# Kernel tuning notes

Measured on AMD Instinct MI355X. Metric: run time of the kernel, lower is better.

## Reference

```python
import jax, jax.numpy as jnp
import numpy as np

N, E = 25000, 400000
IN, HID, OUT = 128, 256, 128
T = 4                      # towers
F1, F2 = HID // T, OUT // T  # per-tower out dims (divide_input=False)
A = 12                     # len(aggregators)=4 * len(scalers)=3
EPS_STD = 1e-5
EPS_BN = 1e-5


def _glorot(k, shape):
    fin, fout = shape[-2], shape[-1]
    lim = float(np.sqrt(6.0 / (fin + fout)))
    return jax.random.uniform(k, shape, jnp.float32, -lim, lim)


def setup_inputs():
    key = jax.random.key(0)
    ks = jax.random.split(key, 10)
    x = jax.random.normal(ks[0], (N, IN), jnp.float32)
    edge_index = jax.random.randint(ks[1], (2, E), 0, N, dtype=jnp.int32)
    # avg_deg['log'] buffer of PNAConv: mean over nodes of log(deg+1)
    deg = jax.ops.segment_sum(jnp.ones((E,), jnp.float32), edge_index[1], num_segments=N)
    avg_log = jnp.mean(jnp.log(deg + 1.0)).astype(jnp.float32)
    return dict(
        x=x, edge_index=edge_index, avg_log=avg_log,
        pre1_W=_glorot(ks[2], (T, 2 * IN, F1)), pre1_b=jnp.zeros((T, F1), jnp.float32),
        post1_W=_glorot(ks[3], (T, IN + A * F1, F1)), post1_b=jnp.zeros((T, F1), jnp.float32),
        lin1_W=_glorot(ks[4], (T * F1, HID)), lin1_b=jnp.zeros((HID,), jnp.float32),
        bn1_g=jnp.ones((HID,), jnp.float32), bn1_b=jnp.zeros((HID,), jnp.float32),
        pre2_W=_glorot(ks[5], (T, 2 * HID, F2)), pre2_b=jnp.zeros((T, F2), jnp.float32),
        post2_W=_glorot(ks[6], (T, HID + A * F2, F2)), post2_b=jnp.zeros((T, F2), jnp.float32),
        lin2_W=_glorot(ks[7], (T * F2, OUT)), lin2_b=jnp.zeros((OUT,), jnp.float32),
        bn2_g=jnp.ones((OUT,), jnp.float32), bn2_b=jnp.zeros((OUT,), jnp.float32),
    )


def _pna(x, src, tgt, preW, preB, postW, postB, linW, linB, avg_log):
    """PNAConv: towers=T, divide_input=False, pre_layers=post_layers=1,
    aggregators [mean,min,max,std], scalers [identity,amplification,attenuation]."""
    n = x.shape[0]
    # message: per tower Linear on concat([x_i, x_j]) where i=target, j=source
    h = jnp.concatenate([x[tgt], x[src]], axis=-1)            # [E, 2*F_in]
    msg = jnp.einsum('ec,tcf->etf', h, preW) + preB           # [E, T, F]
    ones = jnp.ones((msg.shape[0],), msg.dtype)
    deg = jax.ops.segment_sum(ones, tgt, num_segments=n)      # in-degree [n]
    degc = jnp.maximum(deg, 1.0)[:, None, None]
    s1 = jax.ops.segment_sum(msg, tgt, num_segments=n)
    mean = s1 / degc
    s2 = jax.ops.segment_sum(msg * msg, tgt, num_segments=n)
    var = jnp.maximum(s2 / degc - mean * mean, 0.0)
    std = jnp.sqrt(var + EPS_STD)
    has = (deg > 0.0)[:, None, None]
    mn = jnp.where(has, jax.ops.segment_min(msg, tgt, num_segments=n), 0.0)
    mx = jnp.where(has, jax.ops.segment_max(msg, tgt, num_segments=n), 0.0)
    agg = jnp.concatenate([mean, mn, mx, std], axis=-1)       # [n, T, 4F]
    dlog = jnp.log(jnp.maximum(deg, 1.0) + 1.0)[:, None, None]
    out = jnp.concatenate([agg, agg * (dlog / avg_log), agg * (avg_log / dlog)], axis=-1)  # [n, T, 12F]
    xt = jnp.broadcast_to(x[:, None, :], (n, T, x.shape[-1]))
    post_in = jnp.concatenate([xt, out], axis=-1)             # [n, T, F_in + 12F]
    post = jnp.einsum('ntc,tcf->ntf', post_in, postW) + postB # [n, T, F]
    return post.reshape(n, -1) @ linW + linB                  # [n, out]


def _bn(x, g, b):
    # BatchNorm1d training-mode math: biased batch variance
    m = jnp.mean(x, axis=0)
    v = jnp.mean((x - m) ** 2, axis=0)
    return g * (x - m) / jnp.sqrt(v + EPS_BN) + b


def reference(x, edge_index, avg_log, pre1_W, pre1_b, post1_W, post1_b, lin1_W, lin1_b,
              bn1_g, bn1_b, pre2_W, pre2_b, post2_W, post2_b, lin2_W, lin2_b, bn2_g, bn2_b):
    src, tgt = edge_index[0], edge_index[1]
    h = _pna(x, src, tgt, pre1_W, pre1_b, post1_W, post1_b, lin1_W, lin1_b, avg_log)
    h = jax.nn.relu(_bn(jnp.nan_to_num(h), bn1_g, bn1_b))
    h = _pna(h, src, tgt, pre2_W, pre2_b, post2_W, post2_b, lin2_W, lin2_b, avg_log)
    h = jax.nn.relu(_bn(jnp.nan_to_num(h), bn2_g, bn2_b))
    return h
```

## Files before the change

kernel.cpp:

```cpp
#include <hip/hip_runtime.h>
#include <hip/hip_bf16.h>
#include <float.h>
#include <math.h>

typedef __hip_bfloat16 bf16;
typedef __attribute__((ext_vector_type(8))) short short8;
typedef __attribute__((ext_vector_type(4))) float f32x4;

__device__ __forceinline__ float bf2f(bf16 v){ return __bfloat162float(v); }
__device__ __forceinline__ void stv(float* p, float v){ *p = v; }
__device__ __forceinline__ void stv(bf16* p, float v){ *p = __float2bfloat16(v); }
__device__ __forceinline__ float nanfix(float v){
  if (v != v) return 0.f;
  return fminf(fmaxf(v, -FLT_MAX), FLT_MAX);
}
__device__ __forceinline__ unsigned short f2bu(float f){
  unsigned u = __float_as_uint(f);
  unsigned r = u + 0x7FFFu + ((u>>16)&1u);
  return (unsigned short)(r>>16);
}
template<int VEC>
__device__ __forceinline__ void ldbf(const bf16* p, float (&o)[VEC]){
  if constexpr (VEC==4){
    ushort4 r = *(const ushort4*)p;
    o[0]=__uint_as_float((unsigned)r.x<<16); o[1]=__uint_as_float((unsigned)r.y<<16);
    o[2]=__uint_as_float((unsigned)r.z<<16); o[3]=__uint_as_float((unsigned)r.w<<16);
  } else {
    ushort2 r = *(const ushort2*)p;
    o[0]=__uint_as_float((unsigned)r.x<<16); o[1]=__uint_as_float((unsigned)r.y<<16);
  }
}

__global__ void k_scan1(const int* __restrict__ deg, int* __restrict__ bsum, int N){
  __shared__ int sm[256];
  int i = blockIdx.x*256 + threadIdx.x;
  sm[threadIdx.x] = (i < N) ? deg[i] : 0;
  __syncthreads();
  for (int off = 128; off > 0; off >>= 1){
    if (threadIdx.x < off) sm[threadIdx.x] += sm[threadIdx.x + off];
    __syncthreads();
  }
  if (threadIdx.x == 0) bsum[blockIdx.x] = sm[0];
}

__global__ void k_scan2(int* __restrict__ bsum, int NB){
  __shared__ int sm[1024];
  int tid = threadIdx.x;
  sm[tid] = (tid < NB) ? bsum[tid] : 0;
  __syncthreads();
  for (int off = 1; off < 1024; off <<= 1){
    int t = (tid >= off) ? sm[tid-off] : 0;
    __syncthreads();
    sm[tid] += t;
    __syncthreads();
  }
  if (tid < NB) bsum[tid] = (tid == 0) ? 0 : sm[tid-1];
}

__global__ void k_scan3(const int* __restrict__ deg, const int* __restrict__ bsum,
                        int* __restrict__ offs, int N){
  __shared__ int sm[256];
  int tid = threadIdx.x;
  int i = blockIdx.x*256 + tid;
  int v = (i < N) ? deg[i] : 0;
  sm[tid] = v; __syncthreads();
  for (int off = 1; off < 256; off <<= 1){
    int t = (tid >= off) ? sm[tid-off] : 0;
    __syncthreads();
    sm[tid] += t;
    __syncthreads();
  }
  if (i < N) offs[i+1] = bsum[blockIdx.x] + sm[tid];
  if (i == 0) offs[0] = 0;
}

__global__ void k_scatter(const int* __restrict__ src, const int* __restrict__ tgt,
                          const int* __restrict__ offs, int* __restrict__ cnt,
                          int* __restrict__ ssrc, int E){
  int e = blockIdx.x*blockDim.x + threadIdx.x;
  if (e < E){
    int t = tgt[e];
    int pos = offs[t] + atomicAdd(&cnt[t], 1);
    ssrc[pos] = src[e];
  }
}

__device__ __forceinline__ void rp_pqT(const float* preW, const float* preB,
                                       bf16* WpqT, float* bpq, int K, int F, int idx){
  int NC = 4*F;
  int total = 2*NC*K;
  if (idx < total){
    int j = idx/K, c = idx%K;
    int half = j/NC, jj = j%NC, t = jj/F, f = jj%F;
    WpqT[idx] = __float2bfloat16(preW[(t*2*K + half*K + c)*F + f]);
  }
  if (idx < 2*NC) bpq[idx] = (idx < NC) ? preB[idx] : 0.f;
}
__device__ __forceinline__ void rp_xT(const float* postW, const float* postB,
                                      bf16* WxT, float* bpost, int KX, int F, int idx){
  int NC = 4*F; int KP = KX + 12*F;
  if (idx < NC*KX){
    int j = idx/KX, c = idx%KX, t = j/F, f = j%F;
    WxT[idx] = __float2bfloat16(postW[(t*KP + c)*F + f]);
  }
  if (idx < NC) bpost[idx] = postB[idx];
}
__device__ __forceinline__ void rp_agg3(const float* postW, bf16* Wagg3,
                                        int KX, int F, int idx){
  int K4F = 4*F; int KP = KX + 12*F;
  int total = 4*3*F*K4F;
  if (idx < total){
    int k = idx % K4F; int r = idx / K4F;
    int zr = r % (3*F); int t = r / (3*F);
    int s = zr / F, f = zr % F;
    Wagg3[idx] = __float2bfloat16(postW[((size_t)(t*KP + KX + s*K4F + k))*F + f]);
  }
}
__device__ __forceinline__ void rp_linT(const float* linW, bf16* WlinT,
                                        int K, int NC, int idx){
  if (idx < NC*K){
    int j = idx/K, c = idx%K;
    WlinT[idx] = __float2bfloat16(linW[c*NC + j]);
  }
}

struct SetupArgs {
  const float *pre1W, *pre1b, *post1W, *post1b, *lin1W;
  const float *pre2W, *pre2b, *post2W, *post2b, *lin2W;
  const float *x;
  const int *tgt;
  bf16 *WpqT1, *WxT1, *Wagg31, *lin1WT;
  bf16 *WpqT2, *WxT2, *Wagg32, *lin2WT;
  bf16 *x_bf;
  int *deg;
  float *bpq1, *bpost1, *bpq2, *bpost2;
  int nx4;
  int E;
  int gstride;
};

__global__ void k_setup(SetupArgs a){
  int idx = blockIdx.x*256 + threadIdx.x;
  switch (blockIdx.y){
    case 0: rp_pqT (a.pre1W, a.pre1b, a.WpqT1, a.bpq1, 128, 64, idx); break;
    case 1: rp_xT  (a.post1W, a.post1b, a.WxT1, a.bpost1, 128, 64, idx); break;
    case 2: rp_agg3(a.post1W, a.Wagg31, 128, 64, idx); break;
    case 3: rp_linT(a.lin1W, a.lin1WT, 256, 256, idx); break;
    case 4: rp_pqT (a.pre2W, a.pre2b, a.WpqT2, a.bpq2, 256, 32, idx); break;
    case 5: rp_xT  (a.post2W, a.post2b, a.WxT2, a.bpost2, 256, 32, idx); break;
    case 6: rp_agg3(a.post2W, a.Wagg32, 256, 32, idx); break;
    case 7: rp_linT(a.lin2W, a.lin2WT, 128, 128, idx); break;
    case 8:
      for (int i = idx; i < a.nx4; i += a.gstride){
        float4 v = *(const float4*)(a.x + (size_t)i*4);
        ushort4 o = make_ushort4(f2bu(v.x), f2bu(v.y), f2bu(v.z), f2bu(v.w));
        *(ushort4*)(a.x_bf + (size_t)i*4) = o;
      }
      break;
    case 9:
      for (int e = idx; e < a.E; e += a.gstride)
        atomicAdd(&a.deg[a.tgt[e]], 1);
      break;
  }
}

template<typename TO, bool STATS>
__global__ __launch_bounds__(256) void k_mgemm(
    const bf16* __restrict__ A, int lda,
    const bf16* __restrict__ Bt,
    const float* __restrict__ bias,
    TO* __restrict__ Cout, int ldc,
    int N, int K, int NC, float* __restrict__ part)
{
  __shared__ __align__(16) bf16 As[64*40];
  __shared__ __align__(16) bf16 Bs[64*40];
  __shared__ float sstat[4][2][16][2];
  int n0 = blockIdx.y*64;
  int j0 = blockIdx.x*64;
  int tid = threadIdx.x;
  int srow = tid>>2, skoff = (tid&3)*8;
  int wave = tid>>6, lane = tid&63;
  int wy = (wave>>1)*32, wx = (wave&1)*32;
  int l15 = lane&15, q = lane>>4;
  f32x4 acc[2][2] = {};
  for (int k0 = 0; k0 < K; k0 += 32){
    uint4 av = {0,0,0,0};
    int ar = n0 + srow;
    if (ar < N) av = *(const uint4*)(A + (size_t)ar*lda + k0 + skoff);
    *(uint4*)&As[srow*40 + skoff] = av;
    uint4 bv = {0,0,0,0};
    int br = j0 + srow;
    if (br < NC) bv = *(const uint4*)(Bt + (size_t)br*K + k0 + skoff);
    *(uint4*)&Bs[srow*40 + skoff] = bv;
    __syncthreads();
    short8 af[2], bfr[2];
    #pragma unroll
    for (int i = 0; i < 2; i++){
      af[i]  = *(const short8*)&As[(wy + i*16 + l15)*40 + q*8];
      bfr[i] = *(const short8*)&Bs[(wx + i*16 + l15)*40 + q*8];
    }
    #pragma unroll
    for (int mi = 0; mi < 2; mi++)
      #pragma unroll
      for (int ni = 0; ni < 2; ni++)
        acc[mi][ni] = __builtin_amdgcn_mfma_f32_16x16x32_bf16(af[mi], bfr[ni], acc[mi][ni], 0, 0, 0);
    __syncthreads();
  }
  float cs[2] = {0.f, 0.f}, cq[2] = {0.f, 0.f};
  #pragma unroll
  for (int mi = 0; mi < 2; mi++){
    #pragma unroll
    for (int ni = 0; ni < 2; ni++){
      #pragma unroll
      for (int r = 0; r < 4; r++){
        int n  = n0 + wy + mi*16 + q*4 + r;
        int jj = j0 + wx + ni*16 + l15;
        if (n < N && jj < NC){
          float v = acc[mi][ni][r] + bias[jj];
          stv(&Cout[(size_t)n*ldc + jj], v);
          if constexpr (STATS){ cs[ni] += v; cq[ni] = fmaf(v, v, cq[ni]); }
        }
      }
    }
  }
  if constexpr (STATS){
    #pragma unroll
    for (int ni = 0; ni < 2; ni++){
      float s = cs[ni], qq = cq[ni];
      s  += __shfl_xor(s, 16);  s  += __shfl_xor(s, 32);
      qq += __shfl_xor(qq, 16); qq += __shfl_xor(qq, 32);
      if (q == 0){ sstat[wave][ni][l15][0] = s; sstat[wave][ni][l15][1] = qq; }
    }
    __syncthreads();
    if (tid < 64){
      int j = tid;
      int wa = (j < 32) ? 0 : 1, wb = wa + 2;
      int ni = (j & 31) >> 4, li = j & 15;
      float s  = sstat[wa][ni][li][0] + sstat[wb][ni][li][0];
      float qq = sstat[wa][ni][li][1] + sstat[wb][ni][li][1];
      part[(size_t)blockIdx.y*2*ldc + (j0 + j)]       = s;
      part[(size_t)blockIdx.y*2*ldc + ldc + (j0 + j)] = qq;
    }
  }
}

template<int COLS>
__global__ __launch_bounds__(256) void k_postagg(
    const bf16* __restrict__ agg,
    const bf16* __restrict__ Wagg3,
    const bf16* __restrict__ PQX, int ldq, int cinOff,
    const float* __restrict__ scal,
    bf16* __restrict__ Cout, int ldc, int N)
{
  constexpr int K4F = 4*COLS;
  constexpr int ROWS3 = 3*COLS;
  constexpr int NI = COLS/32;
  constexpr int LDA_AGG = 16*COLS;
  __shared__ __align__(16) bf16 As[64*40];
  __shared__ __align__(16) bf16 Bs[ROWS3*40];
  int z = blockIdx.z;
  int n0 = blockIdx.y*64;
  int tid = threadIdx.x;
  int srow = tid>>2, skoff = (tid&3)*8;
  int wave = tid>>6, lane = tid&63;
  int wy = (wave>>1)*32;
  int wx = (wave&1)*(COLS/2);
  int l15 = lane&15, q = lane>>4;
  f32x4 acc[2][NI][3] = {};
  const bf16* Az = agg + (size_t)z*K4F;
  const bf16* Bz = Wagg3 + (size_t)z*ROWS3*K4F;
  for (int k0 = 0; k0 < K4F; k0 += 32){
    uint4 av = {0,0,0,0};
    int ar = n0 + srow;
    if (ar < N) av = *(const uint4*)(Az + (size_t)ar*LDA_AGG + k0 + skoff);
    *(uint4*)&As[srow*40 + skoff] = av;
    for (int r = srow; r < ROWS3; r += 64){
      uint4 bv = *(const uint4*)(Bz + (size_t)r*K4F + k0 + skoff);
      *(uint4*)&Bs[r*40 + skoff] = bv;
    }
    __syncthreads();
    short8 af[2];
    #pragma unroll
    for (int i = 0; i < 2; i++)
      af[i] = *(const short8*)&As[(wy + i*16 + l15)*40 + q*8];
    #pragma unroll
    for (int s = 0; s < 3; s++){
      #pragma unroll
      for (int ni = 0; ni < NI; ni++){
        short8 bfr = *(const short8*)&Bs[(s*COLS + wx + ni*16 + l15)*40 + q*8];
        #pragma unroll
        for (int mi = 0; mi < 2; mi++)
          acc[mi][ni][s] = __builtin_amdgcn_mfma_f32_16x16x32_bf16(af[mi], bfr, acc[mi][ni][s], 0, 0, 0);
      }
    }
    __syncthreads();
  }
  #pragma unroll
  for (int mi = 0; mi < 2; mi++){
    #pragma unroll
    for (int ni = 0; ni < NI; ni++){
      int jj = wx + ni*16 + l15;
      int jg = z*COLS + jj;
      #pragma unroll
      for (int r = 0; r < 4; r++){
        int n = n0 + wy + mi*16 + q*4 + r;
        if (n < N){
          float s1 = scal[2*n], s2 = scal[2*n+1];
          float cin = bf2f(PQX[(size_t)n*ldq + cinOff + jg]);
          float v = cin + acc[mi][ni][0][r] + s1*acc[mi][ni][1][r] + s2*acc[mi][ni][2][r];
          Cout[(size_t)n*ldc + jg] = __float2bfloat16(v);
        }
      }
    }
  }
}

template<int NC, int F>
__global__ __launch_bounds__(256) void k_agg(const bf16* __restrict__ PQ, int lda,
    const int* __restrict__ ssrc, const int* __restrict__ offs,
    const float* __restrict__ avgp,
    bf16* __restrict__ agg, float* __restrict__ scal, int N){
  constexpr int VEC = NC/64;
  int wave = threadIdx.x>>6, lane = threadIdx.x&63;
  int n = blockIdx.x*4 + wave;
  if (n >= N) return;
  int c0 = lane*VEC;
  float p[VEC];
  ldbf<VEC>(PQ + (size_t)n*lda + c0, p);
  int s0 = offs[n], s1 = offs[n+1];
  float sum[VEC], sq[VEC], mn[VEC], mx[VEC];
  #pragma unroll
  for (int v=0;v<VEC;v++){ sum[v]=0.f; sq[v]=0.f; mn[v]=FLT_MAX; mx[v]=-FLT_MAX; }
  const bf16* Q = PQ + NC + c0;
  int i = s0;
  for (; i+7 < s1; i += 8){
    int se[8];
    #pragma unroll
    for (int u=0;u<8;u++) se[u] = ssrc[i+u];
    float qv[8][VEC];
    #pragma unroll
    for (int u=0;u<8;u++) ldbf<VEC>(Q + (size_t)se[u]*lda, qv[u]);
    #pragma unroll
    for (int u=0;u<8;u++){
      #pragma unroll
      for (int v=0;v<VEC;v++){
        float qq = qv[u][v];
        sum[v] += qq; sq[v] = fmaf(qq,qq,sq[v]);
        mn[v] = fminf(mn[v], qq); mx[v] = fmaxf(mx[v], qq);
      }
    }
  }
  for (; i+3 < s1; i += 4){
    int se[4];
    #pragma unroll
    for (int u=0;u<4;u++) se[u] = ssrc[i+u];
    float qv[4][VEC];
    #pragma unroll
    for (int u=0;u<4;u++) ldbf<VEC>(Q + (size_t)se[u]*lda, qv[u]);
    #pragma unroll
    for (int u=0;u<4;u++){
      #pragma unroll
      for (int v=0;v<VEC;v++){
        float qq = qv[u][v];
        sum[v] += qq; sq[v] = fmaf(qq,qq,sq[v]);
        mn[v] = fminf(mn[v], qq); mx[v] = fmaxf(mx[v], qq);
      }
    }
  }
  for (; i < s1; i++){
    int sa = ssrc[i];
    float qa[VEC];
    ldbf<VEC>(Q + (size_t)sa*lda, qa);
    #pragma unroll
    for (int v=0;v<VEC;v++){
      float qq = qa[v];
      sum[v]+=qq; sq[v]=fmaf(qq,qq,sq[v]); mn[v]=fminf(mn[v],qq); mx[v]=fmaxf(mx[v],qq);
    }
  }
  int deg = s1-s0;
  float degf = (float)deg;
  float degc = fmaxf(degf, 1.f);
  unsigned short um[VEC], un[VEC], ux[VEC], us[VEC];
  #pragma unroll
  for (int v=0;v<VEC;v++){
    float pv = p[v];
    float sum_m = fmaf(degf, pv, sum[v]);
    float sq_m  = sq[v] + 2.f*pv*sum[v] + degf*pv*pv;
    float mean = sum_m/degc;
    float var = fmaxf(sq_m/degc - mean*mean, 0.f);
    float sd = sqrtf(var + 1e-5f);
    float mnv = deg>0 ? pv + mn[v] : 0.f;
    float mxv = deg>0 ? pv + mx[v] : 0.f;
    um[v]=f2bu(mean); un[v]=f2bu(mnv); ux[v]=f2bu(mxv); us[v]=f2bu(sd);
  }
  int t = c0 / F, f0 = c0 % F;
  bf16* base = agg + (size_t)n*4*NC + (size_t)t*4*F + f0;
  if constexpr (VEC==4){
    *(ushort4*)(base)       = make_ushort4(um[0],um[1],um[2],um[3]);
    *(ushort4*)(base + F)   = make_ushort4(un[0],un[1],un[2],un[3]);
    *(ushort4*)(base + 2*F) = make_ushort4(ux[0],ux[1],ux[2],ux[3]);
    *(ushort4*)(base + 3*F) = make_ushort4(us[0],us[1],us[2],us[3]);
  } else {
    *(ushort2*)(base)       = make_ushort2(um[0],um[1]);
    *(ushort2*)(base + F)   = make_ushort2(un[0],un[1]);
    *(ushort2*)(base + 2*F) = make_ushort2(ux[0],ux[1]);
    *(ushort2*)(base + 3*F) = make_ushort2(us[0],us[1]);
  }
  if (lane==0){
    float dlog = logf(degc + 1.f);
    float avg = *avgp;
    scal[2*n]   = dlog/avg;
    scal[2*n+1] = avg/dlog;
  }
}

template<int C>
__global__ __launch_bounds__(256) void k_bn_final(const float* __restrict__ part, int PB,
                                                  float* __restrict__ stats){
  int c = blockIdx.x*256 + threadIdx.x;
  if (c >= 2*C) return;
  int CH = gridDim.y;
  int per = (PB + CH - 1)/CH;
  int p0 = blockIdx.y*per, p1 = min(p0 + per, PB);
  float acc = 0.f;
  int p = p0;
  for (; p+4 <= p1; p += 4){
    acc += part[(size_t)p*2*C + c] + part[(size_t)(p+1)*2*C + c]
         + part[(size_t)(p+2)*2*C + c] + part[(size_t)(p+3)*2*C + c];
  }
  for (; p < p1; p++) acc += part[(size_t)p*2*C + c];
  atomicAdd(&stats[c], acc);
}

template<typename TO, int C>
__global__ void k_bn_apply(const bf16* __restrict__ h, const float* __restrict__ stats,
     const float* __restrict__ g, const float* __restrict__ b,
     TO* __restrict__ out, int N){
  int idx = blockIdx.x*blockDim.x + threadIdx.x;
  if (idx >= N*(C/4)) return;
  int c = (idx % (C/4))*4;
  float fn = (float)N;
  float v[4];
  ldbf<4>(h + (size_t)idx*4, v);
  float r[4];
  #pragma unroll
  for (int k = 0; k < 4; k++){
    float m = stats[c+k]/fn;
    float var = fmaxf(stats[C+c+k]/fn - m*m, 0.f);
    float inv = rsqrtf(var + 1e-5f);
    float vv = nanfix(v[k]);
    r[k] = fmaxf(g[c+k]*(vv - m)*inv + b[c+k], 0.f);
  }
  if constexpr (sizeof(TO) == 4){
    float4 o = {r[0], r[1], r[2], r[3]};
    *(float4*)((float*)out + (size_t)idx*4) = o;
  } else {
    ushort4 o = make_ushort4(f2bu(r[0]), f2bu(r[1]), f2bu(r[2]), f2bu(r[3]));
    *(ushort4*)((bf16*)out + (size_t)idx*4) = o;
  }
}

static inline int cdiv(int a, int b){ return (a + b - 1)/b; }

extern "C" void kernel_launch(void* const* d_in, const int* in_sizes, int n_in,
                              void* d_out, int out_size, void* d_ws, size_t ws_size,
                              hipStream_t stream){
  const int IN = 128, HID = 256, T = 4, F1 = 64, F2 = 32;
  const int N = in_sizes[0]/IN;
  const int E = in_sizes[1]/2;
  const int NC1 = T*F1;
  const int NC2 = T*F2;
  const int LDQ1 = 2*NC1 + NC1;
  const int LDQ2 = 2*NC2 + NC2;

  const float* x      = (const float*)d_in[0];
  const int*   ei     = (const int*)  d_in[1];
  const int*   srcE   = ei;
  const int*   tgtE   = ei + E;
  const float* avgp   = (const float*)d_in[2];
  const float* pre1W  = (const float*)d_in[3];
  const float* pre1b  = (const float*)d_in[4];
  const float* post1W = (const float*)d_in[5];
  const float* post1b = (const float*)d_in[6];
  const float* lin1W  = (const float*)d_in[7];
  const float* lin1b  = (const float*)d_in[8];
  const float* bn1g   = (const float*)d_in[9];
  const float* bn1b   = (const float*)d_in[10];
  const float* pre2W  = (const float*)d_in[11];
  const float* pre2b  = (const float*)d_in[12];
  const float* post2W = (const float*)d_in[13];
  const float* post2b = (const float*)d_in[14];
  const float* lin2W  = (const float*)d_in[15];
  const float* lin2b  = (const float*)d_in[16];
  const float* bn2g   = (const float*)d_in[17];
  const float* bn2b   = (const float*)d_in[18];

  char* w = (char*)d_ws;
  auto alloc = [&](size_t bytes)->void*{
    void* p = (void*)w; w += (bytes + 255) & ~(size_t)255; return p;
  };
  bf16* BT1    = (bf16*)alloc((size_t)LDQ1*IN*2);
  bf16* WpqT1  = BT1;              bf16* WxT1 = BT1 + (size_t)2*NC1*IN;
  float* bias1 = (float*)alloc((size_t)LDQ1*4);
  float* bpq1  = bias1;            float* bpost1 = bias1 + 2*NC1;
  bf16* Wagg31 = (bf16*)alloc((size_t)T*3*F1*4*F1*2);
  bf16* lin1WT = (bf16*)alloc((size_t)HID*NC1*2);
  bf16* BT2    = (bf16*)alloc((size_t)LDQ2*HID*2);
  bf16* WpqT2  = BT2;              bf16* WxT2 = BT2 + (size_t)2*NC2*HID;
  float* bias2 = (float*)alloc((size_t)LDQ2*4);
  float* bpq2  = bias2;            float* bpost2 = bias2 + 2*NC2;
  bf16* Wagg32 = (bf16*)alloc((size_t)T*3*F2*4*F2*2);
  bf16* lin2WT = (bf16*)alloc((size_t)128*NC2*2);
  int* deg_i   = (int*)alloc((size_t)N*4);
  int* cnt     = (int*)alloc((size_t)N*4);
  float* stats = (float*)alloc(1024*4);
  size_t zbytes = (size_t)((char*)stats - (char*)deg_i) + 1024*4;
  int* offs    = (int*)alloc((size_t)(N+1)*4);
  int* bsum    = (int*)alloc((size_t)cdiv(N,256)*4);
  int* ssrc    = (int*)alloc((size_t)E*4);
  bf16* x_bf   = (bf16*)alloc((size_t)N*IN*2);
  bf16* PQX    = (bf16*)alloc((size_t)N*LDQ1*2);
  bf16* aggb   = (bf16*)alloc((size_t)N*4*NC1*2);
  float* scal  = (float*)alloc((size_t)N*2*4);
  bf16* postbb = (bf16*)alloc((size_t)N*256*2);
  bf16* hpre   = (bf16*)alloc((size_t)N*256*2);
  bf16* h1b    = (bf16*)alloc((size_t)N*256*2);
  int NB = cdiv(N,64);
  float* part  = (float*)alloc((size_t)NB*512*4);

  hipMemsetAsync(deg_i, 0, zbytes, stream);

  int sgx = cdiv(T*3*F1*4*F1, 256);
  SetupArgs sa = { pre1W, pre1b, post1W, post1b, lin1W,
                   pre2W, pre2b, post2W, post2b, lin2W,
                   x, tgtE,
                   WpqT1, WxT1, Wagg31, lin1WT,
                   WpqT2, WxT2, Wagg32, lin2WT,
                   x_bf, deg_i,
                   bpq1, bpost1, bpq2, bpost2,
                   N*IN/4, E, sgx*256 };
  k_setup<<<dim3(sgx, 10),256,0,stream>>>(sa);

  int NBs = cdiv(N,256);
  k_scan1<<<NBs,256,0,stream>>>(deg_i, bsum, N);
  k_scan2<<<1,1024,0,stream>>>(bsum, NBs);
  k_scan3<<<NBs,256,0,stream>>>(deg_i, bsum, offs, N);
  k_scatter<<<cdiv(E,256),256,0,stream>>>(srcE, tgtE, offs, cnt, ssrc, E);

  k_mgemm<bf16,false><<<dim3(LDQ1/64,NB),256,0,stream>>>(x_bf, IN, BT1, bias1, PQX, LDQ1, N, IN, LDQ1, nullptr);
  k_agg<256,64><<<cdiv(N,4),256,0,stream>>>(PQX, LDQ1, ssrc, offs, avgp, aggb, scal, N);
  k_postagg<64><<<dim3(1,NB,T),256,0,stream>>>(aggb, Wagg31, PQX, LDQ1, 2*NC1, scal,
                                               postbb, NC1, N);
  k_mgemm<bf16,true><<<dim3(4,NB),256,0,stream>>>(postbb, NC1, lin1WT, lin1b, hpre, HID, N, NC1, HID, part);
  k_bn_final<256><<<dim3(2,4),256,0,stream>>>(part, NB, stats);
  k_bn_apply<bf16,256><<<cdiv(N*64,256),256,0,stream>>>(hpre, stats, bn1g, bn1b, h1b, N);

  k_mgemm<bf16,false><<<dim3(LDQ2/64,NB),256,0,stream>>>(h1b, HID, BT2, bias2, PQX, LDQ2, N, HID, LDQ2, nullptr);
  k_agg<128,32><<<cdiv(N,4),256,0,stream>>>(PQX, LDQ2, ssrc, offs, avgp, aggb, scal, N);
  k_postagg<32><<<dim3(1,NB,T),256,0,stream>>>(aggb, Wagg32, PQX, LDQ2, 2*NC2, scal,
                                               postbb, NC2, N);
  k_mgemm<bf16,true><<<dim3(2,NB),256,0,stream>>>(postbb, NC2, lin2WT, lin2b, hpre, 128, N, NC2, 128, part);
  k_bn_final<128><<<dim3(1,4),256,0,stream>>>(part, NB, stats + 512);
  k_bn_apply<float,128><<<cdiv(N*32,256),256,0,stream>>>(hpre, stats + 512, bn2g, bn2b, (float*)d_out, N);
}
```

Before: 371.2 us.

## Fold BN1 apply into layer-2 GEMM A-load and precompute BN coefficients

Replaces the BN stats reduction plus per-element normalization with a single-block kernel that computes per-channel scale and shift. The first BatchNorm+ReLU is then applied on the fly while loading A tiles in the layer-2 projection GEMM, which removes the h1b intermediate and one full elementwise pass over N×256. The trade-off is a serial one-block reduction over all partials, plus redundant BN math on each A-tile load. The nan_to_num clamping is also dropped from the apply step.

```diff
diff --git a/kernel.cpp b/kernel.cpp
--- a/kernel.cpp
+++ b/kernel.cpp
@@ -164,13 +164,14 @@
   }
 }
 
-template<typename TO, bool STATS>
+template<typename TO, bool STATS, bool BNA>
 __global__ __launch_bounds__(256) void k_mgemm(
     const bf16* __restrict__ A, int lda,
     const bf16* __restrict__ Bt,
     const float* __restrict__ bias,
     TO* __restrict__ Cout, int ldc,
-    int N, int K, int NC, float* __restrict__ part)
+    int N, int K, int NC, float* __restrict__ part,
+    const float* __restrict__ bnA, const float* __restrict__ bnB)
 {
   __shared__ __align__(16) bf16 As[64*40];
   __shared__ __align__(16) bf16 Bs[64*40];
@@ -186,7 +187,19 @@
   for (int k0 = 0; k0 < K; k0 += 32){
     uint4 av = {0,0,0,0};
     int ar = n0 + srow;
-    if (ar < N) av = *(const uint4*)(A + (size_t)ar*lda + k0 + skoff);
+    if (ar < N){
+      av = *(const uint4*)(A + (size_t)ar*lda + k0 + skoff);
+      if constexpr (BNA){
+        unsigned short* u = (unsigned short*)&av;
+        #pragma unroll
+        for (int j = 0; j < 8; j++){
+          int ch = k0 + skoff + j;
+          float f = __uint_as_float((unsigned)u[j]<<16);
+          f = fmaxf(fmaf(bnA[ch], f, bnB[ch]), 0.f);
+          u[j] = f2bu(f);
+        }
+      }
+    }
     *(uint4*)&As[srow*40 + skoff] = av;
     uint4 bv = {0,0,0,0};
     int br = j0 + srow;
@@ -415,42 +428,45 @@
 }
 
 template<int C>
-__global__ __launch_bounds__(256) void k_bn_final(const float* __restrict__ part, int PB,
-                                                  float* __restrict__ stats){
-  int c = blockIdx.x*256 + threadIdx.x;
-  if (c >= 2*C) return;
-  int CH = gridDim.y;
-  int per = (PB + CH - 1)/CH;
-  int p0 = blockIdx.y*per, p1 = min(p0 + per, PB);
-  float acc = 0.f;
-  int p = p0;
-  for (; p+4 <= p1; p += 4){
-    acc += part[(size_t)p*2*C + c] + part[(size_t)(p+1)*2*C + c]
-         + part[(size_t)(p+2)*2*C + c] + part[(size_t)(p+3)*2*C + c];
-  }
-  for (; p < p1; p++) acc += part[(size_t)p*2*C + c];
-  atomicAdd(&stats[c], acc);
+__global__ __launch_bounds__(256) void k_bn_coef(const float* __restrict__ part, int PB,
+                                                 const float* __restrict__ g,
+                                                 const float* __restrict__ b,
+                                                 float* __restrict__ coef, int N){
+  int c = threadIdx.x;
+  if (c >= C) return;
+  float s = 0.f, q = 0.f;
+  int p = 0;
+  for (; p+4 <= PB; p += 4){
+    s += part[(size_t)p*2*C + c] + part[(size_t)(p+1)*2*C + c]
+       + part[(size_t)(p+2)*2*C + c] + part[(size_t)(p+3)*2*C + c];
+    q += part[(size_t)p*2*C + C + c] + part[(size_t)(p+1)*2*C + C + c]
+       + part[(size_t)(p+2)*2*C + C + c] + part[(size_t)(p+3)*2*C + C + c];
+  }
+  for (; p < PB; p++){
+    s += part[(size_t)p*2*C + c];
+    q += part[(size_t)p*2*C + C + c];
+  }
+  float fn = (float)N;
+  float m = s/fn;
+  float var = fmaxf(q/fn - m*m, 0.f);
+  float inv = rsqrtf(var + 1e-5f);
+  float a = g[c]*inv;
+  coef[c]     = a;
+  coef[C + c] = b[c] - m*a;
 }
 
 template<typename TO, int C>
-__global__ void k_bn_apply(const bf16* __restrict__ h, const float* __restrict__ stats,
-     const float* __restrict__ g, const float* __restrict__ b,
+__global__ void k_bn_apply(const bf16* __restrict__ h, const float* __restrict__ coef,
      TO* __restrict__ out, int N){
   int idx = blockIdx.x*blockDim.x + threadIdx.x;
   if (idx >= N*(C/4)) return;
   int c = (idx % (C/4))*4;
-  float fn = (float)N;
   float v[4];
   ldbf<4>(h + (size_t)idx*4, v);
   float r[4];
   #pragma unroll
-  for (int k = 0; k < 4; k++){
-    float m = stats[c+k]/fn;
-    float var = fmaxf(stats[C+c+k]/fn - m*m, 0.f);
-    float inv = rsqrtf(var + 1e-5f);
-    float vv = nanfix(v[k]);
-    r[k] = fmaxf(g[c+k]*(vv - m)*inv + b[c+k], 0.f);
-  }
+  for (int k = 0; k < 4; k++)
+    r[k] = fmaxf(fmaf(coef[c+k], v[k], coef[C+c+k]), 0.f);
   if constexpr (sizeof(TO) == 4){
     float4 o = {r[0], r[1], r[2], r[3]};
     *(float4*)((float*)out + (size_t)idx*4) = o;
@@ -513,8 +529,8 @@
   bf16* lin2WT = (bf16*)alloc((size_t)128*NC2*2);
   int* deg_i   = (int*)alloc((size_t)N*4);
   int* cnt     = (int*)alloc((size_t)N*4);
-  float* stats = (float*)alloc(1024*4);
-  size_t zbytes = (size_t)((char*)stats - (char*)deg_i) + 1024*4;
+  size_t zbytes = (size_t)((char*)cnt - (char*)deg_i) + (size_t)N*4;
+  float* coef  = (float*)alloc(1024*4);
   int* offs    = (int*)alloc((size_t)(N+1)*4);
   int* bsum    = (int*)alloc((size_t)cdiv(N,256)*4);
   int* ssrc    = (int*)alloc((size_t)E*4);
@@ -524,7 +540,6 @@
   float* scal  = (float*)alloc((size_t)N*2*4);
   bf16* postbb = (bf16*)alloc((size_t)N*256*2);
   bf16* hpre   = (bf16*)alloc((size_t)N*256*2);
-  bf16* h1b    = (bf16*)alloc((size_t)N*256*2);
   int NB = cdiv(N,64);
   float* part  = (float*)alloc((size_t)NB*512*4);
 
@@ -547,19 +562,22 @@
   k_scan3<<<NBs,256,0,stream>>>(deg_i, bsum, offs, N);
   k_scatter<<<cdiv(E,256),256,0,stream>>>(srcE, tgtE, offs, cnt, ssrc, E);
 
-  k_mgemm<bf16,false><<<dim3(LDQ1/64,NB),256,0,stream>>>(x_bf, IN, BT1, bias1, PQX, LDQ1, N, IN, LDQ1, nullptr);
+  k_mgemm<bf16,false,false><<<dim3(LDQ1/64,NB),256,0,stream>>>(
+      x_bf, IN, BT1, bias1, PQX, LDQ1, N, IN, LDQ1, nullptr, nullptr, nullptr);
   k_agg<256,64><<<cdiv(N,4),256,0,stream>>>(PQX, LDQ1, ssrc, offs, avgp, aggb, scal, N);
   k_postagg<64><<<dim3(1,NB,T),256,0,stream>>>(aggb, Wagg31, PQX, LDQ1, 2*NC1, scal,
                                                postbb, NC1, N);
-  k_mgemm<bf16,true><<<dim3(4,NB),256,0,stream>>>(postbb, NC1, lin1WT, lin1b, hpre, HID, N, NC1, HID, part);
-  k_bn_final<256><<<dim3(2,4),256,0,stream>>>(part, NB, stats);
-  k_bn_apply<bf16,256><<<cdiv(N*64,256),256,0,stream>>>(hpre, stats, bn1g, bn1b, h1b, N);
-
-  k_mgemm<bf16,false><<<dim3(LDQ2/64,NB),256,0,stream>>>(h1b, HID, BT2, bias2, PQX, LDQ2, N, HID, LDQ2, nullptr);
+  k_mgemm<bf16,true,false><<<dim3(4,NB),256,0,stream>>>(
+      postbb, NC1, lin1WT, lin1b, hpre, HID, N, NC1, HID, part, nullptr, nullptr);
+  k_bn_coef<256><<<1,256,0,stream>>>(part, NB, bn1g, bn1b, coef, N);
+
+  k_mgemm<bf16,false,true><<<dim3(LDQ2/64,NB),256,0,stream>>>(
+      hpre, HID, BT2, bias2, PQX, LDQ2, N, HID, LDQ2, nullptr, coef, coef + 256);
   k_agg<128,32><<<cdiv(N,4),256,0,stream>>>(PQX, LDQ2, ssrc, offs, avgp, aggb, scal, N);
   k_postagg<32><<<dim3(1,NB,T),256,0,stream>>>(aggb, Wagg32, PQX, LDQ2, 2*NC2, scal,
                                                postbb, NC2, N);
-  k_mgemm<bf16,true><<<dim3(2,NB),256,0,stream>>>(postbb, NC2, lin2WT, lin2b, hpre, 128, N, NC2, 128, part);
-  k_bn_final<128><<<dim3(1,4),256,0,stream>>>(part, NB, stats + 512);
-  k_bn_apply<float,128><<<cdiv(N*32,256),256,0,stream>>>(hpre, stats + 512, bn2g, bn2b, (float*)d_out, N);
-}
+  k_mgemm<bf16,true,false><<<dim3(2,NB),256,0,stream>>>(
+      postbb, NC2, lin2WT, lin2b, hpre, 128, N, NC2, 128, part, nullptr, nullptr);
+  k_bn_coef<128><<<1,128,0,stream>>>(part, NB, bn2g, bn2b, coef + 512, N);
+  k_bn_apply<float,128><<<cdiv(N*32,256),256,0,stream>>>(hpre, coef + 512, (float*)d_out, N);
+}
```

Result: slower. 412.8 us (+11.2%).
